# Kernel optimization log

Measured on AMD Instinct MI355X. Metric: run time of the kernel, lower is better.

The kernel has to match this reference:

```python
import jax, jax.numpy as jnp
import numpy as np


def setup_inputs() -> dict:
    key = jax.random.key(0)
    k1, k2, k3, k4 = jax.random.split(key, 4)
    N, F, E = 100000, 128, 1600000
    Fo = F // 2
    x = jax.random.normal(k1, (N, F), dtype=jnp.float32)
    edge_index = jax.random.randint(k2, (2, E), 0, N, dtype=jnp.int32)
    W_conv = jax.random.normal(k3, (Fo, F), dtype=jnp.float32) * (1.0 / np.sqrt(F))
    b_conv = jnp.zeros((Fo,), dtype=jnp.float32)
    W_lin = jax.random.normal(k4, (1, Fo), dtype=jnp.float32) * (1.0 / np.sqrt(Fo))
    b_lin = jnp.zeros((1,), dtype=jnp.float32)
    return {"x": x, "edge_index": edge_index, "W_conv": W_conv,
            "b_conv": b_conv, "W_lin": W_lin, "b_lin": b_lin}


def gcn_conv(x, edge_index, W_conv, b_conv):
    # PyG GCNConv: add self-loops, symmetric normalization, x@W.T, scatter-add, + bias
    N = x.shape[0]
    loops = jnp.arange(N, dtype=edge_index.dtype)
    src = jnp.concatenate([edge_index[0], loops])  # message sources
    dst = jnp.concatenate([edge_index[1], loops])  # aggregation targets
    h = x @ W_conv.T  # [N, Fo]
    deg = jax.ops.segment_sum(jnp.ones_like(dst, dtype=h.dtype), dst, num_segments=N)
    dinv = jnp.where(deg > 0, jax.lax.rsqrt(deg), 0.0)
    norm = dinv[src] * dinv[dst]  # [E+N]
    msg = h[src] * norm[:, None]  # [E+N, Fo] -- dominant memory traffic
    agg = jax.ops.segment_sum(msg, dst, num_segments=N)
    return agg + b_conv


def reference(x, edge_index, W_conv, b_conv, W_lin, b_lin):
    h = gcn_conv(x, edge_index, W_conv, b_conv)
    h = jax.nn.relu(h)
    logits = h @ W_lin.T + b_lin  # [N, 1]
    return jax.nn.sigmoid(logits)
```

## Files before the change

### kernel.cpp

```cpp
#include <hip/hip_runtime.h>
#include <math.h>

#define F_IN   128
#define F_OUT  64
#define CHUNK  5120
#define MAXB   512

typedef short bf16x8 __attribute__((ext_vector_type(8)));
typedef float f32x4  __attribute__((ext_vector_type(4)));

__device__ __forceinline__ float bf2f(unsigned short u) {
    union { unsigned int i; float f; } c; c.i = ((unsigned int)u) << 16; return c.f;
}
__device__ __forceinline__ unsigned short f2bf(float f) {
    union { float f; unsigned int i; } c; c.f = f;
    unsigned int r = c.i + 0x7FFFu + ((c.i >> 16) & 1u);
    return (unsigned short)(r >> 16);
}

__global__ __launch_bounds__(256) void k_hist(
    const int* __restrict__ dst, int E, int* __restrict__ M, int NBLK, int NBC) {
    __shared__ int hist[MAXB];
    for (int c = threadIdx.x; c < MAXB; c += 256) hist[c] = 0;
    __syncthreads();
    int e0 = blockIdx.x * CHUNK;
    int e1 = min(E, e0 + CHUNK);
    for (int e = e0 + threadIdx.x; e < e1; e += 256)
        atomicAdd(&hist[dst[e] >> 8], 1);
    __syncthreads();
    for (int c = threadIdx.x; c < NBC; c += 256)
        M[c * NBLK + blockIdx.x] = hist[c];
}

__global__ void k_scan1(const int* __restrict__ M, int* __restrict__ tmp,
                        int* __restrict__ bsum, int S) {
    __shared__ int sh[256];
    int i = blockIdx.x * 256 + threadIdx.x;
    int v = (i < S) ? M[i] : 0;
    sh[threadIdx.x] = v;
    __syncthreads();
    for (int off = 1; off < 256; off <<= 1) {
        int t = (threadIdx.x >= off) ? sh[threadIdx.x - off] : 0;
        __syncthreads();
        sh[threadIdx.x] += t;
        __syncthreads();
    }
    if (i < S) tmp[i] = sh[threadIdx.x];
    if (threadIdx.x == 255) bsum[blockIdx.x] = sh[255];
}

__global__ void k_scan2(int* __restrict__ bsum, int NB1) {
    __shared__ int sh[512];
    int v = (threadIdx.x < NB1) ? bsum[threadIdx.x] : 0;
    sh[threadIdx.x] = v;
    __syncthreads();
    for (int off = 1; off < 512; off <<= 1) {
        int t = (threadIdx.x >= off) ? sh[threadIdx.x - off] : 0;
        __syncthreads();
        sh[threadIdx.x] += t;
        __syncthreads();
    }
    if (threadIdx.x < NB1) bsum[threadIdx.x] = sh[threadIdx.x] - v;
}

__global__ void k_scan3(int* __restrict__ M, const int* __restrict__ tmp,
                        const int* __restrict__ bsum, int* __restrict__ bucketOff,
                        int* __restrict__ offsets,
                        int S, int NBLK, int NBC, int N, int E) {
    int i = blockIdx.x * 256 + threadIdx.x;
    if (i < S) {
        int orig = M[i];
        int o = tmp[i] - orig + bsum[blockIdx.x];
        M[i] = o;
        if (i % NBLK == 0) bucketOff[i / NBLK] = o;
    }
    if (i == 0) { bucketOff[NBC] = E; offsets[N] = E; }
}

__global__ __launch_bounds__(256) void k_scatter(
    const int* __restrict__ src, const int* __restrict__ dst, int E,
    const int* __restrict__ M, int NBLK, int NBC, unsigned int* __restrict__ entries) {
    __shared__ int cur[MAXB];
    for (int c = threadIdx.x; c < NBC; c += 256)
        cur[c] = M[c * NBLK + blockIdx.x];
    __syncthreads();
    int e0 = blockIdx.x * CHUNK;
    int e1 = min(E, e0 + CHUNK);
    for (int e = e0 + threadIdx.x; e < e1; e += 256) {
        int d = dst[e];
        int s = src[e];
        int p = atomicAdd(&cur[d >> 8], 1);
        entries[p] = ((unsigned int)(d & 255) << 24) | (unsigned int)s;
    }
}

__global__ __launch_bounds__(256) void k_sort(
    const unsigned int* __restrict__ entries, const int* __restrict__ bucketOff,
    int* __restrict__ offsets, int* __restrict__ srcs, int N) {
    __shared__ int hist[256];
    __shared__ int curs[256];
    const int tid = threadIdx.x;
    const int b = blockIdx.x;
    const int start = bucketOff[b];
    const int end   = bucketOff[b + 1];

    hist[tid] = 0;
    __syncthreads();
    for (int i = start + tid; i < end; i += 256)
        atomicAdd(&hist[entries[i] >> 24], 1);
    __syncthreads();

    int cntv = hist[tid];
    curs[tid] = cntv;
    __syncthreads();
    for (int off = 1; off < 256; off <<= 1) {
        int t = (tid >= off) ? curs[tid - off] : 0;
        __syncthreads();
        curs[tid] += t;
        __syncthreads();
    }
    int excl = curs[tid] - cntv;
    int d = (b << 8) + tid;
    if (d < N) offsets[d] = start + excl;
    __syncthreads();
    curs[tid] = start + excl;
    __syncthreads();

    for (int i = start + tid; i < end; i += 256) {
        unsigned int v = entries[i];
        int p = atomicAdd(&curs[v >> 24], 1);
        srcs[p] = (int)(v & 0xFFFFFFu);
    }
}

__global__ __launch_bounds__(256) void k_gemm(
    const float* __restrict__ x, const float* __restrict__ W,
    const int* __restrict__ offsets, unsigned short* __restrict__ g, int N) {
    __shared__ unsigned short xs[64 * F_IN];
    __shared__ unsigned short Wsh[F_OUT * F_IN];
    __shared__ float dinvs[64];

    const int tid  = threadIdx.x;
    const int row0 = blockIdx.x * 64;

    {
        const float4* W4 = (const float4*)W;
        #pragma unroll
        for (int t = 0; t < 8; ++t) {
            int idx = t * 256 + tid;
            float4 v = W4[idx];
            ushort4 u;
            u.x = f2bf(v.x); u.y = f2bf(v.y); u.z = f2bf(v.z); u.w = f2bf(v.w);
            *(ushort4*)&Wsh[idx * 4] = u;
        }
    }
    {
        const float4* x4 = (const float4*)x;
        #pragma unroll
        for (int t = 0; t < 8; ++t) {
            int idx = t * 256 + tid;
            int r = idx >> 5;
            int grow = row0 + r;
            float4 v = make_float4(0.f, 0.f, 0.f, 0.f);
            if (grow < N) v = x4[(size_t)grow * 32 + (idx & 31)];
            ushort4 u;
            u.x = f2bf(v.x); u.y = f2bf(v.y); u.z = f2bf(v.z); u.w = f2bf(v.w);
            *(ushort4*)&xs[idx * 4] = u;
        }
    }
    if (tid < 64) {
        int grow = row0 + tid;
        float dv = 1.0f;
        if (grow < N) dv = rsqrtf((float)(offsets[grow + 1] - offsets[grow]) + 1.0f);
        dinvs[tid] = dv;
    }
    __syncthreads();

    const int lane = tid & 63;
    const int wave = tid >> 6;
    const int m = lane & 15;
    const int q = lane >> 4;
    const int r0 = wave * 16;

    bf16x8 a[4];
    #pragma unroll
    for (int ks = 0; ks < 4; ++ks)
        a[ks] = *(const bf16x8*)&xs[(r0 + m) * F_IN + ks * 32 + q * 8];

    f32x4 acc[4] = {{0,0,0,0},{0,0,0,0},{0,0,0,0},{0,0,0,0}};
    #pragma unroll
    for (int ct = 0; ct < 4; ++ct) {
        #pragma unroll
        for (int ks = 0; ks < 4; ++ks) {
            bf16x8 b = *(const bf16x8*)&Wsh[(ct * 16 + m) * F_IN + ks * 32 + q * 8];
            acc[ct] = __builtin_amdgcn_mfma_f32_16x16x32_bf16(a[ks], b, acc[ct], 0, 0, 0);
        }
    }

    float dv[4];
    #pragma unroll
    for (int reg = 0; reg < 4; ++reg)
        dv[reg] = dinvs[r0 + q * 4 + reg];
    #pragma unroll
    for (int ct = 0; ct < 4; ++ct) {
        #pragma unroll
        for (int reg = 0; reg < 4; ++reg) {
            int grow = row0 + r0 + q * 4 + reg;
            if (grow < N)
                g[(size_t)grow * F_OUT + ct * 16 + m] = f2bf(acc[ct][reg] * dv[reg]);
        }
    }
}

__global__ __launch_bounds__(256) void k_pull(
    const unsigned short* __restrict__ g, const int* __restrict__ offsets,
    const int* __restrict__ srcs, const float* __restrict__ b_conv,
    const float* __restrict__ W_lin, const float* __restrict__ b_lin,
    float* __restrict__ out, int N) {
    const int lane   = threadIdx.x & 63;
    const int li     = lane & 31;
    const int half   = lane >> 5;
    const int wave   = (blockIdx.x * blockDim.x + threadIdx.x) >> 6;
    const int nwaves = (gridDim.x * blockDim.x) >> 6;

    const float2 wl = ((const float2*)W_lin)[li];
    const float2 bb = ((const float2*)b_conv)[li];
    const float  bl = b_lin[0];
    const unsigned int* g32 = (const unsigned int*)g;

    for (int i = wave; i < N; i += nwaves) {
        int e0 = __builtin_amdgcn_readfirstlane(offsets[i]);
        int e1 = __builtin_amdgcn_readfirstlane(offsets[i + 1]);

        unsigned int us = g32[(size_t)i * 32 + li];
        float a0 = half ? 0.f : bf2f((unsigned short)(us & 0xFFFFu));
        float a1 = half ? 0.f : bf2f((unsigned short)(us >> 16));

        int e = e0;
        int M16 = e0 + ((e1 - e0) & ~15);
        for (; e < M16; e += 16) {
            unsigned int u[8];
            #pragma unroll
            for (int t = 0; t < 8; ++t) {
                int sA = srcs[e + 2 * t];
                int sB = srcs[e + 2 * t + 1];
                int s  = half ? sB : sA;
                u[t] = g32[(size_t)s * 32 + li];
            }
            #pragma unroll
            for (int t = 0; t < 8; ++t) {
                a0 += bf2f((unsigned short)(u[t] & 0xFFFFu));
                a1 += bf2f((unsigned short)(u[t] >> 16));
            }
        }
        for (; e + 2 <= e1; e += 2) {
            int sA = srcs[e];
            int sB = srcs[e + 1];
            int s  = half ? sB : sA;
            unsigned int u = g32[(size_t)s * 32 + li];
            a0 += bf2f((unsigned short)(u & 0xFFFFu));
            a1 += bf2f((unsigned short)(u >> 16));
        }
        if (e < e1 && half == 0) {
            int s = srcs[e];
            unsigned int u = g32[(size_t)s * 32 + li];
            a0 += bf2f((unsigned short)(u & 0xFFFFu));
            a1 += bf2f((unsigned short)(u >> 16));
        }

        a0 += __shfl_xor(a0, 32, 64);
        a1 += __shfl_xor(a1, 32, 64);

        float dinv = rsqrtf((float)(e1 - e0) + 1.0f);
        float r0 = fmaxf(a0 * dinv + bb.x, 0.f);
        float r1 = fmaxf(a1 * dinv + bb.y, 0.f);
        float t = r0 * wl.x + r1 * wl.y;
        #pragma unroll
        for (int off = 32; off > 0; off >>= 1)
            t += __shfl_down(t, off, 64);
        if (lane == 0)
            out[i] = 1.0f / (1.0f + expf(-(0.5f * t + bl)));
    }
}

extern "C" void kernel_launch(void* const* d_in, const int* in_sizes, int n_in,
                              void* d_out, int out_size, void* d_ws, size_t ws_size,
                              hipStream_t stream) {
    const float* x      = (const float*)d_in[0];
    const int*   ei     = (const int*)d_in[1];
    const float* W_conv = (const float*)d_in[2];
    const float* b_conv = (const float*)d_in[3];
    const float* W_lin  = (const float*)d_in[4];
    const float* b_lin  = (const float*)d_in[5];

    const int N = in_sizes[0] / F_IN;
    const int E = in_sizes[1] / 2;
    const int* src = ei;
    const int* dst = ei + E;
    float* out = (float*)d_out;

    const int NBC  = (N + 255) >> 8;
    const int NBLK = (E + CHUNK - 1) / CHUNK;
    const int S    = NBC * NBLK;
    const int NB1  = (S + 255) / 256;

    const int Na = (N + 256) & ~255;
    const int Sa = (S + 256) & ~255;
    const int Ea = (E + 255) & ~255;

    int* M         = (int*)d_ws;
    int* tmp       = M + Sa;
    int* bsum      = tmp + Sa;
    int* bucketOff = bsum + 512;
    int* offsets   = bucketOff + ((NBC + 257) & ~255);
    unsigned int* entries = (unsigned int*)(offsets + Na);
    int* srcs      = (int*)(entries + Ea);
    unsigned short* g = (unsigned short*)(srcs + Ea);

    k_hist   <<<NBLK, 256, 0, stream>>>(dst, E, M, NBLK, NBC);
    k_scan1  <<<NB1, 256, 0, stream>>>(M, tmp, bsum, S);
    k_scan2  <<<1, 512, 0, stream>>>(bsum, NB1);
    k_scan3  <<<NB1, 256, 0, stream>>>(M, tmp, bsum, bucketOff, offsets, S, NBLK, NBC, N, E);
    k_scatter<<<NBLK, 256, 0, stream>>>(src, dst, E, M, NBLK, NBC, entries);
    k_sort   <<<NBC, 256, 0, stream>>>(entries, bucketOff, offsets, srcs, N);
    k_gemm   <<<(N + 63) / 64, 256, 0, stream>>>(x, W_conv, offsets, g, N);
    k_pull   <<<4096, 256, 0, stream>>>(g, offsets, srcs, b_conv, W_lin, b_lin, out, N);
}
```

Measured before the change: 198.2 us.

## Pad CSR neighbor lists to multiples of 16 with a zero dummy row

The sort kernel now pads each destination's neighbor list to a multiple of 16 using a dummy source index N. The GEMM writes a zero row for N because x is zero-filled past the end. The pull kernel then runs only the unrolled 16-edge loop and drops the scalar remainder loops, and degree is stored separately. This removes tail-loop divergence and instruction overhead, at the cost of extra gathers of the dummy row, a larger padded srcs buffer and a serial pad fill per thread. GEMM bf16 packing also switches to a packed intrinsic conversion.

```diff
diff --git a/kernel.cpp b/kernel.cpp
--- a/kernel.cpp
+++ b/kernel.cpp
@@ -1,10 +1,12 @@
 #include <hip/hip_runtime.h>
+#include <hip/hip_bf16.h>
 #include <math.h>
 
 #define F_IN   128
 #define F_OUT  64
 #define CHUNK  5120
 #define MAXB   512
+#define PADSLACK 4096
 
 typedef short bf16x8 __attribute__((ext_vector_type(8)));
 typedef float f32x4  __attribute__((ext_vector_type(4)));
@@ -16,6 +18,10 @@
     union { float f; unsigned int i; } c; c.f = f;
     unsigned int r = c.i + 0x7FFFu + ((c.i >> 16) & 1u);
     return (unsigned short)(r >> 16);
+}
+__device__ __forceinline__ unsigned int pk2bf(float a, float b) {
+    __hip_bfloat162 p = __float22bfloat162_rn(make_float2(a, b));
+    union { __hip_bfloat162 h; unsigned int u; } c; c.h = p; return c.u;
 }
 
 __global__ __launch_bounds__(256) void k_hist(
@@ -65,8 +71,7 @@
 
 __global__ void k_scan3(int* __restrict__ M, const int* __restrict__ tmp,
                         const int* __restrict__ bsum, int* __restrict__ bucketOff,
-                        int* __restrict__ offsets,
-                        int S, int NBLK, int NBC, int N, int E) {
+                        int S, int NBLK, int NBC, int E) {
     int i = blockIdx.x * 256 + threadIdx.x;
     if (i < S) {
         int orig = M[i];
@@ -74,7 +79,7 @@
         M[i] = o;
         if (i % NBLK == 0) bucketOff[i / NBLK] = o;
     }
-    if (i == 0) { bucketOff[NBC] = E; offsets[N] = E; }
+    if (i == 0) bucketOff[NBC] = E;
 }
 
 __global__ __launch_bounds__(256) void k_scatter(
@@ -96,13 +101,15 @@
 
 __global__ __launch_bounds__(256) void k_sort(
     const unsigned int* __restrict__ entries, const int* __restrict__ bucketOff,
-    int* __restrict__ offsets, int* __restrict__ srcs, int N) {
+    int* __restrict__ offsetsP, int* __restrict__ deg,
+    int* __restrict__ srcsP, int N) {
     __shared__ int hist[256];
     __shared__ int curs[256];
     const int tid = threadIdx.x;
     const int b = blockIdx.x;
     const int start = bucketOff[b];
     const int end   = bucketOff[b + 1];
+    const int startP = start + b * PADSLACK;
 
     hist[tid] = 0;
     __syncthreads();
@@ -110,8 +117,9 @@
         atomicAdd(&hist[entries[i] >> 24], 1);
     __syncthreads();
 
-    int cntv = hist[tid];
-    curs[tid] = cntv;
+    int cntv   = hist[tid];
+    int padded = (cntv + 15) & ~15;
+    curs[tid] = padded;
     __syncthreads();
     for (int off = 1; off < 256; off <<= 1) {
         int t = (tid >= off) ? curs[tid - off] : 0;
@@ -119,23 +127,28 @@
         curs[tid] += t;
         __syncthreads();
     }
-    int excl = curs[tid] - cntv;
+    int exclP = curs[tid] - padded;
     int d = (b << 8) + tid;
-    if (d < N) offsets[d] = start + excl;
-    __syncthreads();
-    curs[tid] = start + excl;
+    if (d < N) { offsetsP[d] = startP + exclP; deg[d] = cntv; }
+    __syncthreads();
+    curs[tid] = startP + exclP;
     __syncthreads();
 
     for (int i = start + tid; i < end; i += 256) {
         unsigned int v = entries[i];
         int p = atomicAdd(&curs[v >> 24], 1);
-        srcs[p] = (int)(v & 0xFFFFFFu);
-    }
+        srcsP[p] = (int)(v & 0xFFFFFFu);
+    }
+    __syncthreads();
+
+    int padEnd = startP + exclP + padded;
+    for (int p = curs[tid]; p < padEnd; ++p)
+        srcsP[p] = N;
 }
 
 __global__ __launch_bounds__(256) void k_gemm(
     const float* __restrict__ x, const float* __restrict__ W,
-    const int* __restrict__ offsets, unsigned short* __restrict__ g, int N) {
+    const int* __restrict__ deg, unsigned short* __restrict__ g, int N) {
     __shared__ unsigned short xs[64 * F_IN];
     __shared__ unsigned short Wsh[F_OUT * F_IN];
     __shared__ float dinvs[64];
@@ -149,9 +162,8 @@
         for (int t = 0; t < 8; ++t) {
             int idx = t * 256 + tid;
             float4 v = W4[idx];
-            ushort4 u;
-            u.x = f2bf(v.x); u.y = f2bf(v.y); u.z = f2bf(v.z); u.w = f2bf(v.w);
-            *(ushort4*)&Wsh[idx * 4] = u;
+            uint2 u = make_uint2(pk2bf(v.x, v.y), pk2bf(v.z, v.w));
+            *(uint2*)&Wsh[idx * 4] = u;
         }
     }
     {
@@ -163,15 +175,14 @@
             int grow = row0 + r;
             float4 v = make_float4(0.f, 0.f, 0.f, 0.f);
             if (grow < N) v = x4[(size_t)grow * 32 + (idx & 31)];
-            ushort4 u;
-            u.x = f2bf(v.x); u.y = f2bf(v.y); u.z = f2bf(v.z); u.w = f2bf(v.w);
-            *(ushort4*)&xs[idx * 4] = u;
+            uint2 u = make_uint2(pk2bf(v.x, v.y), pk2bf(v.z, v.w));
+            *(uint2*)&xs[idx * 4] = u;
         }
     }
     if (tid < 64) {
         int grow = row0 + tid;
         float dv = 1.0f;
-        if (grow < N) dv = rsqrtf((float)(offsets[grow + 1] - offsets[grow]) + 1.0f);
+        if (grow < N) dv = rsqrtf((float)deg[grow] + 1.0f);
         dinvs[tid] = dv;
     }
     __syncthreads();
@@ -206,17 +217,17 @@
         #pragma unroll
         for (int reg = 0; reg < 4; ++reg) {
             int grow = row0 + r0 + q * 4 + reg;
-            if (grow < N)
+            if (grow <= N)
                 g[(size_t)grow * F_OUT + ct * 16 + m] = f2bf(acc[ct][reg] * dv[reg]);
         }
     }
 }
 
 __global__ __launch_bounds__(256) void k_pull(
-    const unsigned short* __restrict__ g, const int* __restrict__ offsets,
-    const int* __restrict__ srcs, const float* __restrict__ b_conv,
-    const float* __restrict__ W_lin, const float* __restrict__ b_lin,
-    float* __restrict__ out, int N) {
+    const unsigned short* __restrict__ g, const int* __restrict__ offsetsP,
+    const int* __restrict__ deg, const int* __restrict__ srcsP,
+    const float* __restrict__ b_conv, const float* __restrict__ W_lin,
+    const float* __restrict__ b_lin, float* __restrict__ out, int N) {
     const int lane   = threadIdx.x & 63;
     const int li     = lane & 31;
     const int half   = lane >> 5;
@@ -229,21 +240,20 @@
     const unsigned int* g32 = (const unsigned int*)g;
 
     for (int i = wave; i < N; i += nwaves) {
-        int e0 = __builtin_amdgcn_readfirstlane(offsets[i]);
-        int e1 = __builtin_amdgcn_readfirstlane(offsets[i + 1]);
+        int e0 = __builtin_amdgcn_readfirstlane(offsetsP[i]);
+        int dg = __builtin_amdgcn_readfirstlane(deg[i]);
+        int e1 = e0 + ((dg + 15) & ~15);
 
         unsigned int us = g32[(size_t)i * 32 + li];
         float a0 = half ? 0.f : bf2f((unsigned short)(us & 0xFFFFu));
         float a1 = half ? 0.f : bf2f((unsigned short)(us >> 16));
 
-        int e = e0;
-        int M16 = e0 + ((e1 - e0) & ~15);
-        for (; e < M16; e += 16) {
+        for (int e = e0; e < e1; e += 16) {
             unsigned int u[8];
             #pragma unroll
             for (int t = 0; t < 8; ++t) {
-                int sA = srcs[e + 2 * t];
-                int sB = srcs[e + 2 * t + 1];
+                int sA = srcsP[e + 2 * t];
+                int sB = srcsP[e + 2 * t + 1];
                 int s  = half ? sB : sA;
                 u[t] = g32[(size_t)s * 32 + li];
             }
@@ -253,25 +263,11 @@
                 a1 += bf2f((unsigned short)(u[t] >> 16));
             }
         }
-        for (; e + 2 <= e1; e += 2) {
-            int sA = srcs[e];
-            int sB = srcs[e + 1];
-            int s  = half ? sB : sA;
-            unsigned int u = g32[(size_t)s * 32 + li];
-            a0 += bf2f((unsigned short)(u & 0xFFFFu));
-            a1 += bf2f((unsigned short)(u >> 16));
-        }
-        if (e < e1 && half == 0) {
-            int s = srcs[e];
-            unsigned int u = g32[(size_t)s * 32 + li];
-            a0 += bf2f((unsigned short)(u & 0xFFFFu));
-            a1 += bf2f((unsigned short)(u >> 16));
-        }
 
         a0 += __shfl_xor(a0, 32, 64);
         a1 += __shfl_xor(a1, 32, 64);
 
-        float dinv = rsqrtf((float)(e1 - e0) + 1.0f);
+        float dinv = rsqrtf((float)dg + 1.0f);
         float r0 = fmaxf(a0 * dinv + bb.x, 0.f);
         float r1 = fmaxf(a1 * dinv + bb.y, 0.f);
         float t = r0 * wl.x + r1 * wl.y;
@@ -307,22 +303,24 @@
     const int Na = (N + 256) & ~255;
     const int Sa = (S + 256) & ~255;
     const int Ea = (E + 255) & ~255;
+    const int EPa = (E + NBC * PADSLACK + 511) & ~255;
 
     int* M         = (int*)d_ws;
     int* tmp       = M + Sa;
     int* bsum      = tmp + Sa;
     int* bucketOff = bsum + 512;
-    int* offsets   = bucketOff + ((NBC + 257) & ~255);
-    unsigned int* entries = (unsigned int*)(offsets + Na);
-    int* srcs      = (int*)(entries + Ea);
-    unsigned short* g = (unsigned short*)(srcs + Ea);
+    int* offsetsP  = bucketOff + (MAXB + 256);
+    int* deg       = offsetsP + Na;
+    unsigned int* entries = (unsigned int*)(deg + Na);
+    int* srcsP     = (int*)(entries + Ea);
+    unsigned short* g = (unsigned short*)(srcsP + EPa);
 
     k_hist   <<<NBLK, 256, 0, stream>>>(dst, E, M, NBLK, NBC);
     k_scan1  <<<NB1, 256, 0, stream>>>(M, tmp, bsum, S);
     k_scan2  <<<1, 512, 0, stream>>>(bsum, NB1);
-    k_scan3  <<<NB1, 256, 0, stream>>>(M, tmp, bsum, bucketOff, offsets, S, NBLK, NBC, N, E);
+    k_scan3  <<<NB1, 256, 0, stream>>>(M, tmp, bsum, bucketOff, S, NBLK, NBC, E);
     k_scatter<<<NBLK, 256, 0, stream>>>(src, dst, E, M, NBLK, NBC, entries);
-    k_sort   <<<NBC, 256, 0, stream>>>(entries, bucketOff, offsets, srcs, N);
-    k_gemm   <<<(N + 63) / 64, 256, 0, stream>>>(x, W_conv, offsets, g, N);
-    k_pull   <<<4096, 256, 0, stream>>>(g, offsets, srcs, b_conv, W_lin, b_lin, out, N);
-}
+    k_sort   <<<NBC, 256, 0, stream>>>(entries, bucketOff, offsetsP, deg, srcsP, N);
+    k_gemm   <<<(N + 64) / 64, 256, 0, stream>>>(x, W_conv, deg, g, N);
+    k_pull   <<<4096, 256, 0, stream>>>(g, offsetsP, deg, srcsP, b_conv, W_lin, b_lin, out, N);
+}
```

Measured after the change: 193.2 us. 1.03x faster.
